# Kernel optimization log

Hardware: AMD Instinct MI355X
Metric: run time of the kernel (lower is better)

Reference implementation:

```python
import jax, jax.numpy as jnp
import numpy as np

L = 32768
D = 512
H = 4
HD = 128  # head dim


def setup_inputs() -> dict:
    key = jax.random.key(0)
    k1, k2, k3, k4, k5 = jax.random.split(key, 5)
    return {
        "x": jax.random.normal(k1, (L, D), dtype=jnp.float32),
        "in_proj_weight": jax.random.normal(k2, (3 * D, D), dtype=jnp.float32) * 0.02,
        "in_proj_bias": jax.random.normal(k3, (3 * D,), dtype=jnp.float32) * 0.02,
        "out_proj_weight": jax.random.normal(k4, (D, D), dtype=jnp.float32) * 0.02,
        "out_proj_bias": jax.random.normal(k5, (D,), dtype=jnp.float32) * 0.02,
    }


def reference(x, in_proj_weight, in_proj_bias, out_proj_weight, out_proj_bias):
    # single-query cross attention: q from x[:1], k/v from full x
    q = x[:1] @ in_proj_weight[:D].T + in_proj_bias[:D]            # [1, D]
    k = x @ in_proj_weight[D:2 * D].T + in_proj_bias[D:2 * D]      # [L, D]
    v = x @ in_proj_weight[2 * D:].T + in_proj_bias[2 * D:]        # [L, D]

    qh = q.reshape(1, H, HD).transpose(1, 0, 2)   # [H, 1, HD]
    kh = k.reshape(L, H, HD).transpose(1, 2, 0)   # [H, HD, L]
    vh = v.reshape(L, H, HD).transpose(1, 0, 2)   # [H, L, HD]

    scale = 1.0 / jnp.sqrt(jnp.float32(HD))
    dot = jnp.matmul(qh, kh) * scale              # [H, 1, L]
    attn = jax.nn.softmax(dot, axis=-1)           # [H, 1, L]
    out = jnp.matmul(attn, vh)                    # [H, 1, HD]

    out = out.transpose(1, 0, 2).reshape(1, D)    # [1, D]
    return out @ out_proj_weight.T + out_proj_bias
```

## Files before the change

kernel.cpp:

```cpp
#include <hip/hip_runtime.h>


#define DIM   512
#define NH    4
#define HDIM  128
#define SCALE 0.08838834764831845f

#define NB              2048
#define ROWS_PER_BLOCK  16
#define ROWS_PER_WAVE   4
#define NSLOT           8

#define WS_Q     0
#define WS_QKS   512
#define WS_QKB   2560
#define WS_ATTN  2568
#define WS_S     3080
#define WS_XA    3112

__global__ __launch_bounds__(256)
void k_qproj(const float* __restrict__ x, const float* __restrict__ ipw,
             const float* __restrict__ ipb, float* __restrict__ ws) {
  const int g = blockIdx.x * 256 + threadIdx.x;
  if (g < NSLOT * NH * DIM) ws[WS_XA + g] = 0.f;
  if (g < NSLOT * NH)       ws[WS_S + g]  = 0.f;
  if (g < NH * DIM)         ws[WS_QKS + g] = 0.f;

  const int wave = threadIdx.x >> 6, lane = threadIdx.x & 63;
  const int d = blockIdx.x * 4 + wave;
  const float4 xa = *(const float4*)(x + lane * 8);
  const float4 xb = *(const float4*)(x + lane * 8 + 4);
  const float* wr = ipw + (size_t)d * DIM + lane * 8;
  const float4 wa = *(const float4*)wr;
  const float4 wb = *(const float4*)(wr + 4);
  float acc = wa.x*xa.x + wa.y*xa.y + wa.z*xa.z + wa.w*xa.w
            + wb.x*xb.x + wb.y*xb.y + wb.z*xb.z + wb.w*xb.w;
  #pragma unroll
  for (int off = 32; off; off >>= 1) acc += __shfl_xor(acc, off, 64);
  if (lane == 0) ws[WS_Q + d] = acc + ipb[d];
}

__global__ __launch_bounds__(256)
void k_qk(const float* __restrict__ ipw, const float* __restrict__ ipb,
          float* __restrict__ ws) {
  const int wave = threadIdx.x >> 6, lane = threadIdx.x & 63;
  const int W  = blockIdx.x * 4 + wave;
  const int o  = W & 31;
  const int hq = W >> 5;
  const int h  = o >> 3;
  const int col = o * 64 + lane;
  const int dp  = col & 511;
  const float* q = ws + WS_Q + h * HDIM + hq * 32;
  const float* wbase = ipw + (size_t)(DIM + h * HDIM + hq * 32) * DIM + dp;
  float acc = 0.f;
  #pragma unroll 8
  for (int i = 0; i < 32; ++i)
    acc += q[i] * wbase[(size_t)i * DIM];
  atomicAdd(ws + WS_QKS + col, acc * SCALE);

  if (W == 0) {
    #pragma unroll
    for (int hh = 0; hh < NH; ++hh) {
      float v = ws[WS_Q + hh * HDIM + lane]      * ipb[DIM + hh * HDIM + lane]
              + ws[WS_Q + hh * HDIM + 64 + lane] * ipb[DIM + hh * HDIM + 64 + lane];
      #pragma unroll
      for (int off = 32; off; off >>= 1) v += __shfl_xor(v, off, 64);
      if (lane == 0) ws[WS_QKB + hh] = v * SCALE;
    }
  }
}

__global__ __launch_bounds__(256)
void k_main(const float* __restrict__ x, float* __restrict__ ws) {
  const int wave = threadIdx.x >> 6, lane = threadIdx.x & 63;
  const int row0 = blockIdx.x * ROWS_PER_BLOCK + wave * ROWS_PER_WAVE;

  float qk[NH][8], qkb[NH];
  #pragma unroll
  for (int h = 0; h < NH; ++h) {
    const float4 a = *(const float4*)(ws + WS_QKS + h * DIM + lane * 8);
    const float4 b = *(const float4*)(ws + WS_QKS + h * DIM + lane * 8 + 4);
    qk[h][0]=a.x; qk[h][1]=a.y; qk[h][2]=a.z; qk[h][3]=a.w;
    qk[h][4]=b.x; qk[h][5]=b.y; qk[h][6]=b.z; qk[h][7]=b.w;
    qkb[h] = ws[WS_QKB + h];
  }

  float s[NH] = {0.f, 0.f, 0.f, 0.f};
  float xacc[NH][8];
  #pragma unroll
  for (int h = 0; h < NH; ++h)
    #pragma unroll
    for (int j = 0; j < 8; ++j) xacc[h][j] = 0.f;

  const float* xp = x + (size_t)row0 * DIM + lane * 8;
  #pragma unroll
  for (int r = 0; r < ROWS_PER_WAVE; ++r) {
    const float* rp = xp + (size_t)r * DIM;
    const float4 a = *(const float4*)rp;
    const float4 b = *(const float4*)(rp + 4);
    const float xr[8] = {a.x,a.y,a.z,a.w,b.x,b.y,b.z,b.w};
    float d0=0.f,d1=0.f,d2=0.f,d3=0.f;
    #pragma unroll
    for (int j = 0; j < 8; ++j) {
      d0 += qk[0][j]*xr[j]; d1 += qk[1][j]*xr[j];
      d2 += qk[2][j]*xr[j]; d3 += qk[3][j]*xr[j];
    }
    #pragma unroll
    for (int off = 32; off; off >>= 1) {
      d0 += __shfl_xor(d0, off, 64);
      d1 += __shfl_xor(d1, off, 64);
      d2 += __shfl_xor(d2, off, 64);
      d3 += __shfl_xor(d3, off, 64);
    }
    const float w0 = __expf(d0 + qkb[0]);
    const float w1 = __expf(d1 + qkb[1]);
    const float w2 = __expf(d2 + qkb[2]);
    const float w3 = __expf(d3 + qkb[3]);
    s[0] += w0; s[1] += w1; s[2] += w2; s[3] += w3;
    #pragma unroll
    for (int j = 0; j < 8; ++j) {
      xacc[0][j] += w0 * xr[j];
      xacc[1][j] += w1 * xr[j];
      xacc[2][j] += w2 * xr[j];
      xacc[3][j] += w3 * xr[j];
    }
  }

  __shared__ float lds_xa[2][NH * DIM];
  __shared__ float lds_s[4][NH];
  if (wave >= 2) {
    #pragma unroll
    for (int h = 0; h < NH; ++h)
      #pragma unroll
      for (int j = 0; j < 8; ++j)
        lds_xa[wave - 2][h * DIM + lane * 8 + j] = xacc[h][j];
  }
  if (lane == 0) {
    #pragma unroll
    for (int h = 0; h < NH; ++h) lds_s[wave][h] = s[h];
  }
  __syncthreads();
  if (wave < 2) {
    #pragma unroll
    for (int h = 0; h < NH; ++h)
      #pragma unroll
      for (int j = 0; j < 8; ++j)
        lds_xa[wave][h * DIM + lane * 8 + j] += xacc[h][j];
  }
  __syncthreads();

  const int slot = blockIdx.x & (NSLOT - 1);
  if (threadIdx.x < NH) {
    const int h = threadIdx.x;
    atomicAdd(ws + WS_S + slot * NH + h,
              lds_s[0][h] + lds_s[1][h] + lds_s[2][h] + lds_s[3][h]);
  }
  #pragma unroll
  for (int j = 0; j < 8; ++j) {
    const int p = threadIdx.x + 256 * j;
    atomicAdd(ws + WS_XA + slot * (NH * DIM) + p, lds_xa[0][p] + lds_xa[1][p]);
  }
}

__global__ __launch_bounds__(256)
void k_vproj(const float* __restrict__ ipw, const float* __restrict__ ipb,
             float* __restrict__ ws) {
  const int wave = threadIdx.x >> 6, lane = threadIdx.x & 63;
  const int c = blockIdx.x * 4 + wave;
  const int h = c >> 7;
  float xs[8] = {0.f,0.f,0.f,0.f,0.f,0.f,0.f,0.f};
  #pragma unroll
  for (int sl = 0; sl < NSLOT; ++sl) {
    const float* xv = ws + WS_XA + sl * (NH * DIM) + h * DIM + lane * 8;
    const float4 a = *(const float4*)xv;
    const float4 b = *(const float4*)(xv + 4);
    xs[0]+=a.x; xs[1]+=a.y; xs[2]+=a.z; xs[3]+=a.w;
    xs[4]+=b.x; xs[5]+=b.y; xs[6]+=b.z; xs[7]+=b.w;
  }
  float S = 0.f;
  #pragma unroll
  for (int sl = 0; sl < NSLOT; ++sl) S += ws[WS_S + sl * NH + h];

  const float* wr = ipw + (size_t)(2 * DIM + c) * DIM + lane * 8;
  const float4 wa = *(const float4*)wr;
  const float4 wb = *(const float4*)(wr + 4);
  float acc = wa.x*xs[0] + wa.y*xs[1] + wa.z*xs[2] + wa.w*xs[3]
            + wb.x*xs[4] + wb.y*xs[5] + wb.z*xs[6] + wb.w*xs[7];
  #pragma unroll
  for (int off = 32; off; off >>= 1) acc += __shfl_xor(acc, off, 64);
  if (lane == 0)
    ws[WS_ATTN + c] = acc / S + ipb[2 * DIM + c];
}

__global__ __launch_bounds__(256)
void k_oproj(const float* __restrict__ opw, const float* __restrict__ opb,
             const float* __restrict__ ws, float* __restrict__ out) {
  const int wave = threadIdx.x >> 6, lane = threadIdx.x & 63;
  const int i = blockIdx.x * 4 + wave;
  const float4 aa = *(const float4*)(ws + WS_ATTN + lane * 8);
  const float4 ab = *(const float4*)(ws + WS_ATTN + lane * 8 + 4);
  const float* wr = opw + (size_t)i * DIM + lane * 8;
  const float4 wa = *(const float4*)wr;
  const float4 wb = *(const float4*)(wr + 4);
  float acc = wa.x*aa.x + wa.y*aa.y + wa.z*aa.z + wa.w*aa.w
            + wb.x*ab.x + wb.y*ab.y + wb.z*ab.z + wb.w*ab.w;
  #pragma unroll
  for (int off = 32; off; off >>= 1) acc += __shfl_xor(acc, off, 64);
  if (lane == 0) out[i] = acc + opb[i];
}

extern "C" void kernel_launch(void* const* d_in, const int* in_sizes, int n_in,
                              void* d_out, int out_size, void* d_ws, size_t ws_size,
                              hipStream_t stream) {
  const float* x   = (const float*)d_in[0];
  const float* ipw = (const float*)d_in[1];
  const float* ipb = (const float*)d_in[2];
  const float* opw = (const float*)d_in[3];
  const float* opb = (const float*)d_in[4];
  float* out = (float*)d_out;
  float* ws  = (float*)d_ws;

  k_qproj<<<128, 256, 0, stream>>>(x, ipw, ipb, ws);
  k_qk   <<<32,  256, 0, stream>>>(ipw, ipb, ws);
  k_main <<<NB,  256, 0, stream>>>(x, ws);
  k_vproj<<<128, 256, 0, stream>>>(ipw, ipb, ws);
  k_oproj<<<128, 256, 0, stream>>>(opw, opb, ws, out);
}
```

Baseline: 129.8 us.

## Use transpose-reduce across heads and drop softmax-invariant key bias term

The four per-head dot-product butterfly reductions in the main kernel are replaced by a transpose-reduce. Each group of four lanes ends up owning one head, which cuts the number of shuffles and computes one exp per lane instead of four. The q·k-bias term is removed, since a constant per-head shift cancels in softmax. The accumulator layout in LDS is permuted to match, and the number of atomic slots doubles. The k_qk kernel is split finer over twice as many blocks, and k_main gets an occupancy hint. The cost is more complex lane-to-head bookkeeping and larger workspace zeroing.

New measurement: 164.1 us. 1.26x slower.

```diff
diff --git a/kernel.cpp b/kernel.cpp
--- a/kernel.cpp
+++ b/kernel.cpp
@@ -9,22 +9,21 @@
 #define NB              2048
 #define ROWS_PER_BLOCK  16
 #define ROWS_PER_WAVE   4
-#define NSLOT           8
+#define NSLOT           16
 
 #define WS_Q     0
 #define WS_QKS   512
-#define WS_QKB   2560
-#define WS_ATTN  2568
-#define WS_S     3080
-#define WS_XA    3112
+#define WS_ATTN  2560
+#define WS_S     3072
+#define WS_XA    3136
 
 __global__ __launch_bounds__(256)
 void k_qproj(const float* __restrict__ x, const float* __restrict__ ipw,
              const float* __restrict__ ipb, float* __restrict__ ws) {
   const int g = blockIdx.x * 256 + threadIdx.x;
-  if (g < NSLOT * NH * DIM) ws[WS_XA + g] = 0.f;
-  if (g < NSLOT * NH)       ws[WS_S + g]  = 0.f;
-  if (g < NH * DIM)         ws[WS_QKS + g] = 0.f;
+  ws[WS_XA + g] = 0.f;
+  if (g < NSLOT * NH) ws[WS_S + g]   = 0.f;
+  if (g < NH * DIM)   ws[WS_QKS + g] = 0.f;
 
   const int wave = threadIdx.x >> 6, lane = threadIdx.x & 63;
   const int d = blockIdx.x * 4 + wave;
@@ -41,56 +40,44 @@
 }
 
 __global__ __launch_bounds__(256)
-void k_qk(const float* __restrict__ ipw, const float* __restrict__ ipb,
-          float* __restrict__ ws) {
+void k_qk(const float* __restrict__ ipw, float* __restrict__ ws) {
   const int wave = threadIdx.x >> 6, lane = threadIdx.x & 63;
   const int W  = blockIdx.x * 4 + wave;
   const int o  = W & 31;
-  const int hq = W >> 5;
+  const int he = W >> 5;
   const int h  = o >> 3;
   const int col = o * 64 + lane;
   const int dp  = col & 511;
-  const float* q = ws + WS_Q + h * HDIM + hq * 32;
-  const float* wbase = ipw + (size_t)(DIM + h * HDIM + hq * 32) * DIM + dp;
+  const float* q = ws + WS_Q + h * HDIM + he * 16;
+  const float* wbase = ipw + (size_t)(DIM + h * HDIM + he * 16) * DIM + dp;
   float acc = 0.f;
-  #pragma unroll 8
-  for (int i = 0; i < 32; ++i)
+  #pragma unroll
+  for (int i = 0; i < 16; ++i)
     acc += q[i] * wbase[(size_t)i * DIM];
   atomicAdd(ws + WS_QKS + col, acc * SCALE);
-
-  if (W == 0) {
-    #pragma unroll
-    for (int hh = 0; hh < NH; ++hh) {
-      float v = ws[WS_Q + hh * HDIM + lane]      * ipb[DIM + hh * HDIM + lane]
-              + ws[WS_Q + hh * HDIM + 64 + lane] * ipb[DIM + hh * HDIM + 64 + lane];
-      #pragma unroll
-      for (int off = 32; off; off >>= 1) v += __shfl_xor(v, off, 64);
-      if (lane == 0) ws[WS_QKB + hh] = v * SCALE;
-    }
-  }
-}
-
-__global__ __launch_bounds__(256)
+}
+
+__global__ __launch_bounds__(256, 8)
 void k_main(const float* __restrict__ x, float* __restrict__ ws) {
   const int wave = threadIdx.x >> 6, lane = threadIdx.x & 63;
+  const bool b1 = lane & 1, b2 = lane & 2;
   const int row0 = blockIdx.x * ROWS_PER_BLOCK + wave * ROWS_PER_WAVE;
 
-  float qk[NH][8], qkb[NH];
+  float qk[NH][8];
   #pragma unroll
   for (int h = 0; h < NH; ++h) {
     const float4 a = *(const float4*)(ws + WS_QKS + h * DIM + lane * 8);
     const float4 b = *(const float4*)(ws + WS_QKS + h * DIM + lane * 8 + 4);
     qk[h][0]=a.x; qk[h][1]=a.y; qk[h][2]=a.z; qk[h][3]=a.w;
     qk[h][4]=b.x; qk[h][5]=b.y; qk[h][6]=b.z; qk[h][7]=b.w;
-    qkb[h] = ws[WS_QKB + h];
-  }
-
-  float s[NH] = {0.f, 0.f, 0.f, 0.f};
+  }
+
+  float s = 0.f;
   float xacc[NH][8];
   #pragma unroll
-  for (int h = 0; h < NH; ++h)
-    #pragma unroll
-    for (int j = 0; j < 8; ++j) xacc[h][j] = 0.f;
+  for (int i = 0; i < NH; ++i)
+    #pragma unroll
+    for (int j = 0; j < 8; ++j) xacc[i][j] = 0.f;
 
   const float* xp = x + (size_t)row0 * DIM + lane * 8;
   #pragma unroll
@@ -105,18 +92,21 @@
       d0 += qk[0][j]*xr[j]; d1 += qk[1][j]*xr[j];
       d2 += qk[2][j]*xr[j]; d3 += qk[3][j]*xr[j];
     }
-    #pragma unroll
-    for (int off = 32; off; off >>= 1) {
-      d0 += __shfl_xor(d0, off, 64);
-      d1 += __shfl_xor(d1, off, 64);
-      d2 += __shfl_xor(d2, off, 64);
-      d3 += __shfl_xor(d3, off, 64);
-    }
-    const float w0 = __expf(d0 + qkb[0]);
-    const float w1 = __expf(d1 + qkb[1]);
-    const float w2 = __expf(d2 + qkb[2]);
-    const float w3 = __expf(d3 + qkb[3]);
-    s[0] += w0; s[1] += w1; s[2] += w2; s[3] += w3;
+    const float x01 = b1 ? d0 : d1;
+    const float x23 = b1 ? d2 : d3;
+    const float A = (b1 ? d1 : d0) + __shfl_xor(x01, 1, 64);
+    const float B = (b1 ? d3 : d2) + __shfl_xor(x23, 1, 64);
+    const float y = b2 ? A : B;
+    float v = (b2 ? B : A) + __shfl_xor(y, 2, 64);
+    v += __shfl_xor(v, 4, 64);
+    v += __shfl_xor(v, 8, 64);
+    v += __shfl_xor(v, 16, 64);
+    v += __shfl_xor(v, 32, 64);
+    const float w0 = __expf(v);
+    const float w1 = __shfl_xor(w0, 1, 64);
+    const float w2 = __shfl_xor(w0, 2, 64);
+    const float w3 = __shfl_xor(w0, 3, 64);
+    s += w0;
     #pragma unroll
     for (int j = 0; j < 8; ++j) {
       xacc[0][j] += w0 * xr[j];
@@ -128,24 +118,22 @@
 
   __shared__ float lds_xa[2][NH * DIM];
   __shared__ float lds_s[4][NH];
+  const int hbase = lane & 3;
   if (wave >= 2) {
     #pragma unroll
-    for (int h = 0; h < NH; ++h)
+    for (int i = 0; i < NH; ++i)
       #pragma unroll
       for (int j = 0; j < 8; ++j)
-        lds_xa[wave - 2][h * DIM + lane * 8 + j] = xacc[h][j];
-  }
-  if (lane == 0) {
-    #pragma unroll
-    for (int h = 0; h < NH; ++h) lds_s[wave][h] = s[h];
-  }
+        lds_xa[wave - 2][((hbase ^ i) << 9) + lane * 8 + j] = xacc[i][j];
+  }
+  if (lane < NH) lds_s[wave][lane] = s;
   __syncthreads();
   if (wave < 2) {
     #pragma unroll
-    for (int h = 0; h < NH; ++h)
+    for (int i = 0; i < NH; ++i)
       #pragma unroll
       for (int j = 0; j < 8; ++j)
-        lds_xa[wave][h * DIM + lane * 8 + j] += xacc[h][j];
+        lds_xa[wave][((hbase ^ i) << 9) + lane * 8 + j] += xacc[i][j];
   }
   __syncthreads();
 
@@ -221,7 +209,7 @@
   float* ws  = (float*)d_ws;
 
   k_qproj<<<128, 256, 0, stream>>>(x, ipw, ipb, ws);
-  k_qk   <<<32,  256, 0, stream>>>(ipw, ipb, ws);
+  k_qk   <<<64,  256, 0, stream>>>(ipw, ws);
   k_main <<<NB,  256, 0, stream>>>(x, ws);
   k_vproj<<<128, 256, 0, stream>>>(ipw, ipb, ws);
   k_oproj<<<128, 256, 0, stream>>>(opw, opb, ws, out);
```
